# Kernel tuning notes

Measured on AMD Instinct MI355X. Metric: run time of the kernel, lower is better.

Reference implementation:

```python
import jax, jax.numpy as jnp
import numpy as np

B, N, NVT, HS, GS, NZ, TE = 512, 32, 32, 512, 1024, 56, 3


def setup_inputs() -> dict:
    key = jax.random.key(0)
    ks = jax.random.split(key, 18)
    def w(k, shape, fan_in):
        return (jax.random.normal(k, shape, jnp.float32) / np.sqrt(fan_in)).astype(jnp.float32)
    node_types = jax.random.randint(ks[0], (B, N), 0, NVT, dtype=jnp.int32)
    # strictly upper-triangular random DAG: adj[b,u,v]=1 means edge u->v, u<v
    adj = ((jax.random.uniform(ks[1], (B, N, N)) < 0.15)
           & (jnp.triu(jnp.ones((N, N), bool), 1))).astype(jnp.float32)
    return {
        'node_types': node_types,
        'adj': adj,
        'finit_w': w(ks[2], (NVT + GS, HS), NVT + GS),
        'finit_b': w(ks[3], (HS,), HS),
        'fe_w':    w(ks[4], (2 * HS + 1, 2 * HS), 2 * HS + 1),
        'fe_b':    w(ks[5], (2 * HS,), 2 * HS),
        'grue_wih': w(ks[6], (TE, 3 * HS, 2 * HS), 2 * HS),
        'grue_whh': w(ks[7], (TE, 3 * HS, HS), HS),
        'grue_bih': w(ks[8], (TE, 3 * HS), HS),
        'grue_bhh': w(ks[9], (TE, 3 * HS), HS),
        'gate_w':  w(ks[10], (HS, GS), HS),
        'gate_b':  w(ks[11], (GS,), HS),
        'mapper_w': w(ks[12], (HS, GS), HS),
        'fc1_w':   w(ks[13], (GS, NZ), GS),
        'fc1_b':   w(ks[14], (NZ,), GS),
        'fc2_w':   w(ks[15], (GS, NZ), GS),
        'fc2_b':   w(ks[16], (NZ,), GS),
    }


def reference(node_types, adj, finit_w, finit_b, fe_w, fe_b,
              grue_wih, grue_whh, grue_bih, grue_bhh,
              gate_w, gate_b, mapper_w, fc1_w, fc1_b, fc2_w, fc2_b):
    # --- vertex init: finit(cat([one_hot(type), zeros(gs)])) -> only first NVT rows of finit_w matter
    X = jax.nn.one_hot(node_types, NVT, dtype=adj.dtype)          # [B,N,nvt]
    H = X @ finit_w[:NVT] + finit_b                                # [B,N,hs]

    deg = adj.sum(1)                                               # [B,N] in-degree of v
    # torch skips the fe+GRU update for vertex v only if NO graph in batch has a pred at v
    has_pred = (adj.sum((0, 1)) > 0)[None, :, None]                # [1,N,1]

    # fe(cat([H_u, e=1, H_v])) decomposed: W_nei@H_u + w_e + W_self@H_v + b, summed over preds
    Wn, we, Ws = fe_w[:HS], fe_w[HS], fe_w[HS + 1:]

    def step(H, p):
        wih, whh, bih, bhh = p
        Hu = H @ Wn                                                # [B,N,2hs]
        self_t = H @ Ws + we + fe_b                                # [B,N,2hs]
        # Av[b,v] = sum_u adj[b,u,v]*Hu[b,u] + deg[b,v]*self_t[b,v]
        Av = jnp.einsum('buv,bue->bve', adj, Hu) + deg[..., None] * self_t
        gx = Av @ wih.T + bih                                      # [B,N,3hs]
        gh = H @ whh.T + bhh                                       # [B,N,3hs]
        xr, xz, xn = jnp.split(gx, 3, -1)
        hr, hz, hn = jnp.split(gh, 3, -1)
        r = jax.nn.sigmoid(xr + hr)
        z = jax.nn.sigmoid(xz + hz)
        n = jnp.tanh(xn + r * hn)
        Hn = (1.0 - z) * n + z * H                                 # torch GRUCell
        return jnp.where(has_pred, Hn, H), None

    H, _ = jax.lax.scan(step, H, (grue_wih, grue_whh, grue_bih, grue_bhh))

    # gated graph readout: sum_v sigmoid(gate(Hv)) * mapper(Hv)
    Hg = (jax.nn.sigmoid(H @ gate_w + gate_b) * (H @ mapper_w)).sum(1)  # [B,gs]
    mu = Hg @ fc1_w + fc1_b
    logvar = Hg @ fc2_w + fc2_b
    return jnp.stack([mu, logvar], 0)                              # [2,B,nz]
```

## Files before the change

kernel.cpp:

```cpp
#include <hip/hip_runtime.h>
#include <hip/hip_bf16.h>

namespace {

constexpr int kB = 512, kN = 32, kHS = 512, kHS2 = 1024, kHS3 = 1536;
constexpr int kGS = 1024, kNZ = 56, kTE = 3;

typedef __attribute__((ext_vector_type(8))) short bf16x8;
typedef __attribute__((ext_vector_type(4))) float f32x4;

__device__ inline ushort f2bf(float f) {
    union { float f; unsigned u; } v; v.f = f;
    unsigned r = v.u + 0x7fffu + ((v.u >> 16) & 1u);
    return (ushort)(r >> 16);
}
__device__ inline float bf2f(ushort b) {
    union { unsigned u; float f; } v; v.u = ((unsigned)b) << 16;
    return v.f;
}

__global__ __launch_bounds__(256) void wnst_kernel(const float* __restrict__ fe_w,
    ushort* __restrict__ out)
{
    int idx = blockIdx.x * 256 + threadIdx.x;
    int n = idx >> 9, k = idx & 511;
    float v = (n < kHS2) ? fe_w[(size_t)k * kHS2 + n]
                         : fe_w[(size_t)(kHS + 1 + k) * kHS2 + (n - kHS2)];
    out[idx] = f2bf(v);
}

__global__ __launch_bounds__(256) void gatemap_kernel(const float* __restrict__ gw,
    const float* __restrict__ mw, ushort* __restrict__ out)
{
    int idx = blockIdx.x * 256 + threadIdx.x;
    int n = idx >> 9, k = idx & 511;
    float v = (n < kGS) ? gw[(size_t)k * kGS + n] : mw[(size_t)k * kGS + (n - kGS)];
    out[idx] = f2bf(v);
}

__global__ __launch_bounds__(256) void catrzn_kernel(const float* __restrict__ wih,
    const float* __restrict__ whh, ushort* __restrict__ out)
{
    int k = blockIdx.x * 256 + threadIdx.x;
    int n = blockIdx.y, t = blockIdx.z;
    float v;
    if (k < kHS2)       v = wih[((size_t)t * kHS3 + n) * kHS2 + k];
    else if (n < kHS2)  v = whh[((size_t)t * kHS3 + n) * kHS + (k - kHS2)];
    else                v = 0.f;
    out[((size_t)t * kHS3 + n) * kHS3 + k] = f2bf(v);
}

__global__ __launch_bounds__(256) void whhn_kernel(const float* __restrict__ whh,
    ushort* __restrict__ out)
{
    int k = blockIdx.x * 256 + threadIdx.x;
    int n = blockIdx.y, t = blockIdx.z;
    out[((size_t)t * kHS + n) * kHS + k] =
        f2bf(whh[((size_t)t * kHS3 + kHS2 + n) * kHS + k]);
}

__global__ __launch_bounds__(256) void deg_kernel(const float* __restrict__ adj,
    float* __restrict__ deg)
{
    int idx = blockIdx.x * 256 + threadIdx.x;
    int b = idx >> 5, v = idx & 31;
    const float* p = adj + (size_t)b * kN * kN + v;
    float s = 0.f;
    #pragma unroll
    for (int u = 0; u < kN; ++u) s += p[u * kN];
    deg[idx] = s;
}

__global__ void haspred_kernel(const float* __restrict__ deg, int* __restrict__ hp)
{
    int v = threadIdx.x;
    float s = 0.f;
    for (int b = 0; b < kB; ++b) s += deg[b * kN + v];
    hp[v] = (s > 0.f) ? 1 : 0;
}

__global__ void biasHS_kernel(const float* __restrict__ fe_w,
    const float* __restrict__ fe_b, float* __restrict__ o)
{
    int e = blockIdx.x * 256 + threadIdx.x;
    o[e] = (e < kHS2) ? 0.f
                      : fe_w[(size_t)kHS * kHS2 + (e - kHS2)] + fe_b[e - kHS2];
}

__global__ void biasGXN_kernel(const float* __restrict__ bih,
    const float* __restrict__ bhh, float* __restrict__ o)
{
    int idx = blockIdx.x * 256 + threadIdx.x;
    int t = idx / kHS3, e = idx % kHS3;
    float v = bih[t * kHS3 + e];
    if (e < kHS2) v += bhh[t * kHS3 + e];
    o[idx] = v;
}

__global__ void biasRO_kernel(const float* __restrict__ gb, float* __restrict__ o)
{
    int e = blockIdx.x * 256 + threadIdx.x;
    o[e] = (e < kGS) ? gb[e] : 0.f;
}

__global__ __launch_bounds__(256) void hinit_kernel(const int* __restrict__ nt,
    const float* __restrict__ finit_w, const float* __restrict__ finit_b,
    ushort* __restrict__ AvH)
{
    int idx = blockIdx.x * 256 + threadIdx.x;
    int m = idx >> 9;
    int h = idx & 511;
    int t = nt[m];
    AvH[(size_t)m * kHS3 + kHS2 + h] = f2bf(finit_w[t * kHS + h] + finit_b[h]);
}

template<typename CT>
__global__ __launch_bounds__(256) void gemm_bf16(const ushort* __restrict__ A,
    const ushort* __restrict__ B, CT* __restrict__ C,
    const float* __restrict__ bias, int M_, int N_, int K_, int lda)
{
    __shared__ ushort As[128 * 64];
    __shared__ ushort Bs[128 * 64];
    const int tid = threadIdx.x;
    const int w = tid >> 6, l = tid & 63;
    const int mT = blockIdx.y * 128, nT = blockIdx.x * 128;
    const int wm = w >> 1, wn = w & 1;

    f32x4 acc[4][4] = {};

    const int lr = l >> 3;
    const int ls = (l & 7) ^ lr;

    for (int kt = 0; kt < K_; kt += 64) {
        #pragma unroll
        for (int i = 0; i < 4; ++i) {
            int c = w * 4 + i;
            int row = c * 8 + lr;
            const ushort* ga = A + (size_t)(mT + row) * lda + kt + ls * 8;
            __builtin_amdgcn_global_load_lds(
                (const __attribute__((address_space(1))) void*)ga,
                (__attribute__((address_space(3))) void*)(As + c * 512), 16, 0, 0);
            const ushort* gb = B + (size_t)(nT + row) * K_ + kt + ls * 8;
            __builtin_amdgcn_global_load_lds(
                (const __attribute__((address_space(1))) void*)gb,
                (__attribute__((address_space(3))) void*)(Bs + c * 512), 16, 0, 0);
        }
        __syncthreads();

        #pragma unroll
        for (int kk = 0; kk < 2; ++kk) {
            const int s = (kk * 4 + (l >> 4)) ^ (l & 7);
            bf16x8 af[4], bfr[4];
            #pragma unroll
            for (int mi = 0; mi < 4; ++mi) {
                int r = wm * 64 + mi * 16 + (l & 15);
                af[mi] = *reinterpret_cast<const bf16x8*>(&As[r * 64 + s * 8]);
            }
            #pragma unroll
            for (int ni = 0; ni < 4; ++ni) {
                int r = wn * 64 + ni * 16 + (l & 15);
                bfr[ni] = *reinterpret_cast<const bf16x8*>(&Bs[r * 64 + s * 8]);
            }
            #pragma unroll
            for (int mi = 0; mi < 4; ++mi)
                #pragma unroll
                for (int ni = 0; ni < 4; ++ni)
                    acc[mi][ni] = __builtin_amdgcn_mfma_f32_16x16x32_bf16(
                        af[mi], bfr[ni], acc[mi][ni], 0, 0, 0);
        }
        __syncthreads();
    }

    const int col0 = l & 15;
    const int row0 = (l >> 4) * 4;
    #pragma unroll
    for (int ni = 0; ni < 4; ++ni) {
        int col = nT + wn * 64 + ni * 16 + col0;
        float bv = bias ? bias[col] : 0.f;
        #pragma unroll
        for (int mi = 0; mi < 4; ++mi) {
            #pragma unroll
            for (int q = 0; q < 4; ++q) {
                int row = mT + wm * 64 + mi * 16 + row0 + q;
                float val = acc[mi][ni][q] + bv;
                if constexpr (sizeof(CT) == 2)
                    C[(size_t)row * N_ + col] = (CT)f2bf(val);
                else
                    C[(size_t)row * N_ + col] = (CT)val;
            }
        }
    }
}

template<typename CT>
void launch_gemm(const ushort* A, int lda, const ushort* B, CT* C,
                 const float* bias, int M_, int N_, int K_, hipStream_t stream)
{
    dim3 grid(N_ / 128, M_ / 128);
    gemm_bf16<CT><<<grid, 256, 0, stream>>>(A, B, C, bias, M_, N_, K_, lda);
}

__global__ __launch_bounds__(256) void av_kernel(const float* __restrict__ adj,
    const ushort* __restrict__ HuSt, const float* __restrict__ deg,
    ushort* __restrict__ AvH)
{
    __shared__ float adjs[kN * kN];
    __shared__ float degs[kN];
    int b = blockIdx.y;
    int e = blockIdx.x * 256 + threadIdx.x;
    {
        const float4* src = reinterpret_cast<const float4*>(adj + (size_t)b * kN * kN);
        float4 v = src[threadIdx.x];
        *reinterpret_cast<float4*>(&adjs[threadIdx.x * 4]) = v;
        if (threadIdx.x < kN) degs[threadIdx.x] = deg[b * kN + threadIdx.x];
    }
    __syncthreads();

    const size_t rbase = (size_t)b * kN * 2048 + e;
    float acc[kN];
    #pragma unroll
    for (int v = 0; v < kN; ++v)
        acc[v] = degs[v] * bf2f(HuSt[rbase + (size_t)v * 2048 + kHS2]);
    for (int u = 0; u < kN; ++u) {
        float hu = bf2f(HuSt[rbase + (size_t)u * 2048]);
        #pragma unroll
        for (int v4 = 0; v4 < kN / 4; ++v4) {
            float4 a = *reinterpret_cast<const float4*>(&adjs[u * kN + v4 * 4]);
            acc[v4 * 4 + 0] = fmaf(a.x, hu, acc[v4 * 4 + 0]);
            acc[v4 * 4 + 1] = fmaf(a.y, hu, acc[v4 * 4 + 1]);
            acc[v4 * 4 + 2] = fmaf(a.z, hu, acc[v4 * 4 + 2]);
            acc[v4 * 4 + 3] = fmaf(a.w, hu, acc[v4 * 4 + 3]);
        }
    }
    const size_t obase = (size_t)b * kN * kHS3 + e;
    #pragma unroll
    for (int v = 0; v < kN; ++v) AvH[obase + (size_t)v * kHS3] = f2bf(acc[v]);
}

__global__ __launch_bounds__(256) void gru_kernel(ushort* __restrict__ AvH,
    const ushort* __restrict__ gxzn, const ushort* __restrict__ hn,
    const int* __restrict__ hp)
{
    int idx = blockIdx.x * 256 + threadIdx.x;
    int m = idx >> 9;
    int h = idx & 511;
    size_t gb = (size_t)m * kHS3 + h;
    float rp = bf2f(gxzn[gb]);
    float zp = bf2f(gxzn[gb + kHS]);
    float xn = bf2f(gxzn[gb + 2 * kHS]);
    float hv = bf2f(hn[(size_t)m * kHS + h]);
    float r = 1.f / (1.f + __expf(-rp));
    float z = 1.f / (1.f + __expf(-zp));
    float n = tanhf(xn + r * hv);
    ushort* Hp = AvH + (size_t)m * kHS3 + kHS2 + h;
    float hold = bf2f(*Hp);
    float hnew = (1.f - z) * n + z * hold;
    *Hp = hp[m & 31] ? f2bf(hnew) : f2bf(hold);
}

__global__ __launch_bounds__(256) void hg_kernel(const float* __restrict__ G12,
    float* __restrict__ Hg)
{
    int idx = blockIdx.x * 256 + threadIdx.x;
    int b = idx >> 10, g = idx & 1023;
    size_t base = (size_t)b * kN * 2048 + g;
    float acc = 0.f;
    #pragma unroll 8
    for (int n = 0; n < kN; ++n) {
        float s  = G12[base + (size_t)n * 2048];
        float m2 = G12[base + (size_t)n * 2048 + kGS];
        float sig = 1.f / (1.f + __expf(-s));
        acc = fmaf(sig, m2, acc);
    }
    Hg[idx] = acc;
}

__global__ __launch_bounds__(64) void fc_kernel(const float* __restrict__ Hg,
    const float* __restrict__ fc1_w, const float* __restrict__ fc1_b,
    const float* __restrict__ fc2_w, const float* __restrict__ fc2_b,
    float* __restrict__ out, int b0)
{
    __shared__ float hg[kGS];
    int bl = blockIdx.x;
    for (int i = threadIdx.x; i < kGS; i += 64) hg[i] = Hg[(size_t)bl * kGS + i];
    __syncthreads();
    int j = threadIdx.x;
    if (j < kNZ) {
        float s1 = fc1_b[j], s2 = fc2_b[j];
        for (int k = 0; k < kGS; ++k) {
            float h = hg[k];
            s1 = fmaf(h, fc1_w[k * kNZ + j], s1);
            s2 = fmaf(h, fc2_w[k * kNZ + j], s2);
        }
        int bg = b0 + bl;
        out[(size_t)bg * kNZ + j] = s1;
        out[(size_t)kB * kNZ + (size_t)bg * kNZ + j] = s2;
    }
}

}

extern "C" void kernel_launch(void* const* d_in, const int* in_sizes, int n_in,
                              void* d_out, int out_size, void* d_ws, size_t ws_size,
                              hipStream_t stream)
{
    const int*   node_types = (const int*)  d_in[0];
    const float* adj        = (const float*)d_in[1];
    const float* finit_w    = (const float*)d_in[2];
    const float* finit_b    = (const float*)d_in[3];
    const float* fe_w       = (const float*)d_in[4];
    const float* fe_b       = (const float*)d_in[5];
    const float* grue_wih   = (const float*)d_in[6];
    const float* grue_whh   = (const float*)d_in[7];
    const float* grue_bih   = (const float*)d_in[8];
    const float* grue_bhh   = (const float*)d_in[9];
    const float* gate_w     = (const float*)d_in[10];
    const float* gate_b     = (const float*)d_in[11];
    const float* mapper_w   = (const float*)d_in[12];
    const float* fc1_w      = (const float*)d_in[13];
    const float* fc1_b      = (const float*)d_in[14];
    const float* fc2_w      = (const float*)d_in[15];
    const float* fc2_b      = (const float*)d_in[16];
    float* out = (float*)d_out;

    float* W = (float*)d_ws;
    size_t o = 0;
    float*  deg     = W + o; o += (size_t)kB * kN;
    int*    hp      = (int*)(W + o); o += 64;
    float*  biasHS  = W + o; o += 2048;
    float*  biasGXN = W + o; o += kTE * kHS3;
    float*  biasRO  = W + o; o += 2048;
    float*  Hg      = W + o; o += (size_t)kB * kGS;
    ushort* WnsT    = (ushort*)(W + o); o += (size_t)2048 * kHS / 2;
    ushort* catRZN  = (ushort*)(W + o); o += (size_t)kTE * kHS3 * kHS3 / 2;
    ushort* whhN    = (ushort*)(W + o); o += (size_t)kTE * kHS * kHS / 2;
    ushort* gateMapT= (ushort*)(W + o); o += (size_t)2048 * kHS / 2;
    const size_t fixedFloats = o;

    const size_t perGraph = 90112;
    int CH = 512;
    while (CH > 4 &&
           (fixedFloats + (size_t)CH * perGraph) * sizeof(float) > ws_size)
        CH >>= 1;

    deg_kernel<<<kB * kN / 256, 256, 0, stream>>>(adj, deg);
    haspred_kernel<<<1, kN, 0, stream>>>(deg, hp);
    biasHS_kernel<<<2048 / 256, 256, 0, stream>>>(fe_w, fe_b, biasHS);
    biasGXN_kernel<<<kTE * kHS3 / 256, 256, 0, stream>>>(grue_bih, grue_bhh, biasGXN);
    biasRO_kernel<<<2048 / 256, 256, 0, stream>>>(gate_b, biasRO);
    wnst_kernel<<<2048 * kHS / 256, 256, 0, stream>>>(fe_w, WnsT);
    catrzn_kernel<<<dim3(kHS3 / 256, kHS3, kTE), 256, 0, stream>>>(grue_wih, grue_whh, catRZN);
    whhn_kernel<<<dim3(kHS / 256, kHS, kTE), 256, 0, stream>>>(grue_whh, whhN);
    gatemap_kernel<<<2048 * kHS / 256, 256, 0, stream>>>(gate_w, mapper_w, gateMapT);

    for (int b0 = 0; b0 < kB; b0 += CH) {
        const int MC = CH * kN;
        ushort* AvH  = (ushort*)(W + fixedFloats);
        ushort* HuSt = AvH  + (size_t)MC * kHS3;
        ushort* gxzn = HuSt + (size_t)MC * 2048;
        ushort* hnb  = gxzn + (size_t)MC * kHS3;
        float*  G12  = (float*)HuSt;
        ushort* Hc   = AvH + kHS2;

        hinit_kernel<<<MC * kHS / 256, 256, 0, stream>>>(
            node_types + (size_t)b0 * kN, finit_w, finit_b, AvH);

        for (int t = 0; t < kTE; ++t) {
            launch_gemm<ushort>(Hc, kHS3, WnsT, HuSt, biasHS, MC, 2048, kHS, stream);
            {
                dim3 g(kHS2 / 256, CH);
                av_kernel<<<g, 256, 0, stream>>>(
                    adj + (size_t)b0 * kN * kN, HuSt, deg + (size_t)b0 * kN, AvH);
            }
            launch_gemm<ushort>(AvH, kHS3, catRZN + (size_t)t * kHS3 * kHS3, gxzn,
                                biasGXN + t * kHS3, MC, kHS3, kHS3, stream);
            launch_gemm<ushort>(Hc, kHS3, whhN + (size_t)t * kHS * kHS, hnb,
                                grue_bhh + t * kHS3 + kHS2, MC, kHS, kHS, stream);
            gru_kernel<<<MC * kHS / 256, 256, 0, stream>>>(AvH, gxzn, hnb, hp);
        }

        launch_gemm<float>(Hc, kHS3, gateMapT, G12, biasRO, MC, 2048, kHS, stream);
        hg_kernel<<<CH * kGS / 256, 256, 0, stream>>>(G12, Hg);
        fc_kernel<<<CH, 64, 0, stream>>>(Hg, fc1_w, fc1_b, fc2_w, fc2_b, out, b0);
    }
}
```

Measured before the change: 923.0 us.

## Triple-buffer GEMM with 128x256 tiles, split-phase async LDS loads, and block swizzle

Rewrites the bf16 MFMA GEMM main loop to use a three-stage LDS ring buffer with K-step 32. Global-to-LDS loads for tile t+2 are issued in two phases interleaved with the compute halves, gated by explicit vmcnt waits. The output tile grows to 128x256 with each wave owning a 64-column strip, and the grid is swizzled in groups of 8 for L2 locality. It also adds setprio around the MFMA bursts and a launch-bounds occupancy hint. The aim is to hide global load latency and cut barrier stalls, at the cost of more registers and LDS per block and fewer blocks when N is small.

```diff
diff --git a/kernel.cpp b/kernel.cpp
--- a/kernel.cpp
+++ b/kernel.cpp
@@ -115,73 +115,112 @@
 }
 
 template<typename CT>
-__global__ __launch_bounds__(256) void gemm_bf16(const ushort* __restrict__ A,
+__global__ __launch_bounds__(256, 2) void gemm_bf16(const ushort* __restrict__ A,
     const ushort* __restrict__ B, CT* __restrict__ C,
     const float* __restrict__ bias, int M_, int N_, int K_, int lda)
 {
-    __shared__ ushort As[128 * 64];
-    __shared__ ushort Bs[128 * 64];
+    __shared__ ushort smem[3 * 12288];
     const int tid = threadIdx.x;
     const int w = tid >> 6, l = tid & 63;
-    const int mT = blockIdx.y * 128, nT = blockIdx.x * 128;
-    const int wm = w >> 1, wn = w & 1;
-
-    f32x4 acc[4][4] = {};
-
-    const int lr = l >> 3;
-    const int ls = (l & 7) ^ lr;
-
-    for (int kt = 0; kt < K_; kt += 64) {
-        #pragma unroll
-        for (int i = 0; i < 4; ++i) {
-            int c = w * 4 + i;
-            int row = c * 8 + lr;
-            const ushort* ga = A + (size_t)(mT + row) * lda + kt + ls * 8;
-            __builtin_amdgcn_global_load_lds(
-                (const __attribute__((address_space(1))) void*)ga,
-                (__attribute__((address_space(3))) void*)(As + c * 512), 16, 0, 0);
-            const ushort* gb = B + (size_t)(nT + row) * K_ + kt + ls * 8;
-            __builtin_amdgcn_global_load_lds(
-                (const __attribute__((address_space(1))) void*)gb,
-                (__attribute__((address_space(3))) void*)(Bs + c * 512), 16, 0, 0);
-        }
-        __syncthreads();
-
-        #pragma unroll
-        for (int kk = 0; kk < 2; ++kk) {
-            const int s = (kk * 4 + (l >> 4)) ^ (l & 7);
-            bf16x8 af[4], bfr[4];
+    const int l15 = l & 15;
+
+    int nwg = gridDim.x * gridDim.y;
+    int bid = blockIdx.y * gridDim.x + blockIdx.x;
+    int swz = (nwg & 7) ? bid : ((bid & 7) * (nwg >> 3) + (bid >> 3));
+    const int bx = swz % gridDim.x, by = swz / gridDim.x;
+    const int mT = by * 128, nT = bx * 256;
+
+    const int NT = K_ >> 5;
+
+    auto stage = [&](const ushort* G, int ldg, int rowOff, int buf, int aOff,
+                     int idx, int kt2) {
+        int row = idx >> 2, sl = idx & 3;
+        int gs = sl ^ ((row >> 1) & 3);
+        const ushort* g = G + (size_t)(rowOff + row) * ldg + kt2 + gs * 8;
+        __builtin_amdgcn_global_load_lds(
+            (const __attribute__((address_space(1))) void*)g,
+            (__attribute__((address_space(3))) void*)(smem + buf * 12288 + aOff + idx * 8),
+            16, 0, 0);
+    };
+    auto stage_ph0 = [&](int t) {
+        int buf = t % 3, kt2 = t * 32;
+        stage(A, lda, mT, buf, 0, tid, kt2);
+        stage(A, lda, mT, buf, 0, 256 + tid, kt2);
+        stage(B, K_, nT, buf, 4096, tid, kt2);
+    };
+    auto stage_ph1 = [&](int t) {
+        int buf = t % 3, kt2 = t * 32;
+        stage(B, K_, nT, buf, 4096, 256 + tid, kt2);
+        stage(B, K_, nT, buf, 4096, 512 + tid, kt2);
+        stage(B, K_, nT, buf, 4096, 768 + tid, kt2);
+    };
+
+    f32x4 acc[8][4] = {};
+    bf16x8 bfr[4];
+    const int swd = ((l >> 4) ^ (l15 >> 1)) & 3;
+
+    stage_ph0(0); stage_ph1(0);
+    stage_ph0(1); stage_ph1(1);
+
+    for (int t = 0; t < NT; ++t) {
+        if (t + 1 < NT) asm volatile("s_waitcnt vmcnt(6)" ::: "memory");
+        else            asm volatile("s_waitcnt vmcnt(0)" ::: "memory");
+        __builtin_amdgcn_s_barrier();
+
+        const ushort* Ab = smem + (t % 3) * 12288;
+        const ushort* Bb = Ab + 4096;
+        const bool st = (t + 2 < NT);
+
+        bf16x8 af[4];
+        #pragma unroll
+        for (int i = 0; i < 4; ++i)
+            af[i] = *reinterpret_cast<const bf16x8*>(
+                &Ab[(i * 16 + l15) * 32 + swd * 8]);
+        #pragma unroll
+        for (int j = 0; j < 4; ++j)
+            bfr[j] = *reinterpret_cast<const bf16x8*>(
+                &Bb[(w * 64 + j * 16 + l15) * 32 + swd * 8]);
+        if (st) stage_ph0(t + 2);
+        asm volatile("s_waitcnt lgkmcnt(0)" ::: "memory");
+        __builtin_amdgcn_sched_barrier(0);
+        __builtin_amdgcn_s_setprio(1);
+        #pragma unroll
+        for (int i = 0; i < 4; ++i)
             #pragma unroll
-            for (int mi = 0; mi < 4; ++mi) {
-                int r = wm * 64 + mi * 16 + (l & 15);
-                af[mi] = *reinterpret_cast<const bf16x8*>(&As[r * 64 + s * 8]);
-            }
+            for (int j = 0; j < 4; ++j)
+                acc[i][j] = __builtin_amdgcn_mfma_f32_16x16x32_bf16(
+                    af[i], bfr[j], acc[i][j], 0, 0, 0);
+        __builtin_amdgcn_s_setprio(0);
+        __builtin_amdgcn_s_barrier();
+
+        #pragma unroll
+        for (int i = 0; i < 4; ++i)
+            af[i] = *reinterpret_cast<const bf16x8*>(
+                &Ab[((4 + i) * 16 + l15) * 32 + swd * 8]);
+        if (st) stage_ph1(t + 2);
+        asm volatile("s_waitcnt lgkmcnt(0)" ::: "memory");
+        __builtin_amdgcn_sched_barrier(0);
+        __builtin_amdgcn_s_setprio(1);
+        #pragma unroll
+        for (int i = 0; i < 4; ++i)
             #pragma unroll
-            for (int ni = 0; ni < 4; ++ni) {
-                int r = wn * 64 + ni * 16 + (l & 15);
-                bfr[ni] = *reinterpret_cast<const bf16x8*>(&Bs[r * 64 + s * 8]);
-            }
-            #pragma unroll
-            for (int mi = 0; mi < 4; ++mi)
-                #pragma unroll
-                for (int ni = 0; ni < 4; ++ni)
-                    acc[mi][ni] = __builtin_amdgcn_mfma_f32_16x16x32_bf16(
-                        af[mi], bfr[ni], acc[mi][ni], 0, 0, 0);
-        }
-        __syncthreads();
-    }
-
-    const int col0 = l & 15;
+            for (int j = 0; j < 4; ++j)
+                acc[4 + i][j] = __builtin_amdgcn_mfma_f32_16x16x32_bf16(
+                    af[i], bfr[j], acc[4 + i][j], 0, 0, 0);
+        __builtin_amdgcn_s_setprio(0);
+        __builtin_amdgcn_s_barrier();
+    }
+
     const int row0 = (l >> 4) * 4;
     #pragma unroll
     for (int ni = 0; ni < 4; ++ni) {
-        int col = nT + wn * 64 + ni * 16 + col0;
+        int col = nT + w * 64 + ni * 16 + l15;
         float bv = bias ? bias[col] : 0.f;
         #pragma unroll
-        for (int mi = 0; mi < 4; ++mi) {
+        for (int mi = 0; mi < 8; ++mi) {
             #pragma unroll
             for (int q = 0; q < 4; ++q) {
-                int row = mT + wm * 64 + mi * 16 + row0 + q;
+                int row = mT + mi * 16 + row0 + q;
                 float val = acc[mi][ni][q] + bv;
                 if constexpr (sizeof(CT) == 2)
                     C[(size_t)row * N_ + col] = (CT)f2bf(val);
@@ -196,7 +235,7 @@
 void launch_gemm(const ushort* A, int lda, const ushort* B, CT* C,
                  const float* bias, int M_, int N_, int K_, hipStream_t stream)
 {
-    dim3 grid(N_ / 128, M_ / 128);
+    dim3 grid(N_ / 256, M_ / 128);
     gemm_bf16<CT><<<grid, 256, 0, stream>>>(A, B, C, bias, M_, N_, K_, lda);
 }
 
```

New measurement: 870.0 us. 5.7% less time.
